# Performance work log

Hardware: AMD Instinct MI355X
Metric: run time of the kernel (lower is better)

The kernel has to match this reference:

```python
import jax, jax.numpy as jnp
import numpy as np

SR = 4  # search_range
D = 2 * SR + 1  # 9
NC = D * D      # 81 output channels


def setup_inputs() -> dict:
    key = jax.random.key(0)
    k1, k2 = jax.random.split(key)
    B, C, H, W = 8, 64, 192, 256
    x1 = jax.random.normal(k1, (B, C, H, W), dtype=jnp.float32)
    x2 = jax.random.normal(k2, (B, C, H, W), dtype=jnp.float32)
    return {"x1": x1, "x2": x2}


def reference(x1, x2):
    B, C, H, W = x1.shape
    # Zero-pad x2 so out-of-overlap products are zero, matching the
    # zero-initialized cv in the original module.
    x2p = jnp.pad(x2, ((0, 0), (0, 0), (SR, SR), (SR, SR)))
    outs = [None] * NC
    for i in range(-SR, SR + 1):
        for j in range(-SR, SR + 1):
            # Original torch code uses cv[:, 9*i + j] with negative wraparound.
            k = (D * i + j) % NC
            # x2 sample position is (h - i, w - j); in padded coords start = SR - i.
            shifted = jax.lax.dynamic_slice(
                x2p, (0, 0, SR - i, SR - j), (B, C, H, W))
            outs[k] = jnp.sum(x1 * shifted, axis=1)  # [B, H, W]
    cv = jnp.stack(outs, axis=1)  # [B, 81, H, W]
    return cv / NC
```

## Files before the change

kernel.cpp:

```cpp
#include <hip/hip_runtime.h>

#define HH 192
#define WW 256
#define TH 8
#define TW 32
#define CCH 4
#define NCHUNK 16
#define THREADS 576
#define CHSTEP (CCH * HH * WW)

typedef float f4 __attribute__((ext_vector_type(4)));

#define GLL(gp, lp) __builtin_amdgcn_global_load_lds(                        \
    (const __attribute__((address_space(1))) unsigned int*)(gp),            \
    (__attribute__((address_space(3))) unsigned int*)(lp), 16, 0, 0)

__global__ __launch_bounds__(THREADS) void cost_volume_kernel(
    const float* __restrict__ x1, const float* __restrict__ x2,
    float* __restrict__ out)
{
    __shared__ __align__(16) float smem[7168];

    const int tid  = threadIdx.x;
    const int wave = tid >> 6;
    const int lane = tid & 63;
    const int r    = lane >> 3;
    const int wcg  = lane & 7;

    const int bid = blockIdx.x;
    const int b   = bid / 192;
    const int rem = bid % 192;
    const int h0  = (rem >> 3) * TH;
    const int w0  = (rem & 7) * TW;

    const int u2a = tid;
    const int ch2a = u2a / 160, r2a = (u2a % 160) / 10, c2a = (u2a % 10) * 4;
    const int hg2a = h0 - 4 + r2a, wg2a = w0 - 4 + c2a;
    const bool v2a = (hg2a >= 0) & (hg2a < HH) & (wg2a >= 0) & (wg2a <= WW - 4);
    const long off2a = ((long)(b * 64 + ch2a) * HH + hg2a) * WW + wg2a;

    const int u2b = 576 + lane;
    const int ch2b = u2b / 160, r2b = (u2b % 160) / 10, c2b = (u2b % 10) * 4;
    const int hg2b = h0 - 4 + r2b, wg2b = w0 - 4 + c2b;
    const bool v2b = (wave == 0) & (hg2b >= 0) & (hg2b < HH) &
                     (wg2b >= 0) & (wg2b <= WW - 4);
    const long off2b = ((long)(b * 64 + ch2b) * HH + hg2b) * WW + wg2b;

    const bool hx1 = (wave >= 1) & (wave <= 4);
    const int u1 = (64 * (wave - 1) + lane) & 255;
    const int ch1 = u1 >> 6, r1 = (u1 & 63) >> 3, c1 = (u1 & 7) * 4;
    const long off1 = ((long)(b * 64 + ch1) * HH + (h0 + r1)) * WW + (w0 + c1);

    auto issue = [&](int nb, int n) {
        const long cofs = (long)n * CHSTEP;
        float* const l2a = smem + 2048 + nb * 2560 + 256 * wave;
        float* const l2b = smem + 2048 + nb * 2560 + 2304;
        float* const l1  = smem + nb * 1024 + 256 * (wave - 1);
        if (v2a) GLL(x2 + off2a + cofs, l2a);
        if (v2b) GLL(x2 + off2b + cofs, l2b);
        if (hx1) GLL(x1 + off1 + cofs, l1);
    };

    const f4 z4 = {0.f, 0.f, 0.f, 0.f};
    for (int z = tid; z < 7168 / 4; z += THREADS) ((f4*)smem)[z] = z4;
    __syncthreads();

    issue(0, 0);
    __syncthreads();

    f4 acc0 = z4, acc1 = z4, acc2 = z4, acc3 = z4, acc4 = z4,
       acc5 = z4, acc6 = z4, acc7 = z4, acc8 = z4;

    const int row2 = r + 8 - wave;

    for (int n = 0; n < NCHUNK; ++n) {
        if (n + 1 < NCHUNK) issue((n + 1) & 1, n + 1);
        const float* sb1 = smem + (n & 1) * 1024 + r * 32 + wcg * 4;
        const float* sb2 = smem + 2048 + (n & 1) * 2560 + row2 * 40 + wcg * 4;
#pragma unroll
        for (int cc = 0; cc < CCH; ++cc) {
            const f4 av  = *(const f4*)(sb1 + cc * 256);
            const f4 xv0 = *(const f4*)(sb2 + cc * 640);
            const f4 xv1 = *(const f4*)(sb2 + cc * 640 + 4);
            const f4 xv2 = *(const f4*)(sb2 + cc * 640 + 8);
            const f4 w8 = xv0;
            const f4 w7 = __builtin_shufflevector(xv0, xv1, 1, 2, 3, 4);
            const f4 w6 = __builtin_shufflevector(xv0, xv1, 2, 3, 4, 5);
            const f4 w5 = __builtin_shufflevector(xv0, xv1, 3, 4, 5, 6);
            const f4 w4 = xv1;
            const f4 w3 = __builtin_shufflevector(xv1, xv2, 1, 2, 3, 4);
            const f4 w2 = __builtin_shufflevector(xv1, xv2, 2, 3, 4, 5);
            const f4 w1 = __builtin_shufflevector(xv1, xv2, 3, 4, 5, 6);
            const f4 w0 = xv2;
            acc0 = __builtin_elementwise_fma(av, w0, acc0);
            acc1 = __builtin_elementwise_fma(av, w1, acc1);
            acc2 = __builtin_elementwise_fma(av, w2, acc2);
            acc3 = __builtin_elementwise_fma(av, w3, acc3);
            acc4 = __builtin_elementwise_fma(av, w4, acc4);
            acc5 = __builtin_elementwise_fma(av, w5, acc5);
            acc6 = __builtin_elementwise_fma(av, w6, acc6);
            acc7 = __builtin_elementwise_fma(av, w7, acc7);
            acc8 = __builtin_elementwise_fma(av, w8, acc8);
        }
        __syncthreads();
    }

    const float scale = 1.0f / 81.0f;
    const int hout = h0 + r;
    const int wout = w0 + wcg * 4;
#define CV_OUT(JJ)                                                           \
    {                                                                        \
        const int k = (9 * wave + (JJ) + 41) % 81;                           \
        float* po = out + (((long)b * 81 + k) * HH + hout) * WW + wout;      \
        *(f4*)po = acc##JJ * scale;                                          \
    }
    CV_OUT(0) CV_OUT(1) CV_OUT(2) CV_OUT(3) CV_OUT(4)
    CV_OUT(5) CV_OUT(6) CV_OUT(7) CV_OUT(8)
#undef CV_OUT
}

extern "C" void kernel_launch(void* const* d_in, const int* in_sizes, int n_in,
                              void* d_out, int out_size, void* d_ws, size_t ws_size,
                              hipStream_t stream) {
    const float* x1 = (const float*)d_in[0];
    const float* x2 = (const float*)d_in[1];
    float* out = (float*)d_out;
    dim3 grid(8 * 24 * 8);
    dim3 block(THREADS);
    hipLaunchKernelGGL(cost_volume_kernel, grid, block, 0, stream, x1, x2, out);
}
```

Baseline: 120.7 us.

## Load x1 directly into registers and double channel chunk size

Stops staging x1 through LDS; each thread now reads its own x1 float4 straight from global memory into registers, and LDS holds only x2 halos. The channel chunk per pipeline stage doubles from 4 to 8, which halves the number of barriers and enlarges the x2 LDS buffers. This aims to cut LDS traffic and synchronisation overhead. The cost is direct global loads that sit on the compute critical path, plus more LDS per block, which may lower occupancy.

```diff
diff --git a/kernel.cpp b/kernel.cpp
--- a/kernel.cpp
+++ b/kernel.cpp
@@ -4,8 +4,8 @@
 #define WW 256
 #define TH 8
 #define TW 32
-#define CCH 4
-#define NCHUNK 16
+#define CCH 8
+#define NCHUNK 8
 #define THREADS 576
 #define CHSTEP (CCH * HH * WW)
 
@@ -19,7 +19,7 @@
     const float* __restrict__ x1, const float* __restrict__ x2,
     float* __restrict__ out)
 {
-    __shared__ __align__(16) float smem[7168];
+    __shared__ __align__(16) float smem[10240];
 
     const int tid  = threadIdx.x;
     const int wave = tid >> 6;
@@ -33,36 +33,33 @@
     const int h0  = (rem >> 3) * TH;
     const int w0  = (rem & 7) * TW;
 
-    const int u2a = tid;
-    const int ch2a = u2a / 160, r2a = (u2a % 160) / 10, c2a = (u2a % 10) * 4;
-    const int hg2a = h0 - 4 + r2a, wg2a = w0 - 4 + c2a;
-    const bool v2a = (hg2a >= 0) & (hg2a < HH) & (wg2a >= 0) & (wg2a <= WW - 4);
-    const long off2a = ((long)(b * 64 + ch2a) * HH + hg2a) * WW + wg2a;
+    const int uA = tid;
+    const int uB = 576 + tid;
+    const int uC = 1152 + tid;
+    const bool hC = (tid < 128);
 
-    const int u2b = 576 + lane;
-    const int ch2b = u2b / 160, r2b = (u2b % 160) / 10, c2b = (u2b % 10) * 4;
-    const int hg2b = h0 - 4 + r2b, wg2b = w0 - 4 + c2b;
-    const bool v2b = (wave == 0) & (hg2b >= 0) & (hg2b < HH) &
-                     (wg2b >= 0) & (wg2b <= WW - 4);
-    const long off2b = ((long)(b * 64 + ch2b) * HH + hg2b) * WW + wg2b;
-
-    const bool hx1 = (wave >= 1) & (wave <= 4);
-    const int u1 = (64 * (wave - 1) + lane) & 255;
-    const int ch1 = u1 >> 6, r1 = (u1 & 63) >> 3, c1 = (u1 & 7) * 4;
-    const long off1 = ((long)(b * 64 + ch1) * HH + (h0 + r1)) * WW + (w0 + c1);
+    auto desc = [&](int u, bool& v, long& goff) {
+        const int ch = u / 160, row = (u % 160) / 10, c4 = (u % 10) * 4;
+        const int hg = h0 - 4 + row, wg = w0 - 4 + c4;
+        v = (hg >= 0) & (hg < HH) & (wg >= 0) & (wg <= WW - 4);
+        goff = ((long)(b * 64 + ch) * HH + hg) * WW + wg;
+    };
+    bool vA, vB, vC0; long gA, gB, gC;
+    desc(uA, vA, gA);
+    desc(uB, vB, gB);
+    desc(uC, vC0, gC);
+    const bool vC = vC0 & hC;
 
     auto issue = [&](int nb, int n) {
         const long cofs = (long)n * CHSTEP;
-        float* const l2a = smem + 2048 + nb * 2560 + 256 * wave;
-        float* const l2b = smem + 2048 + nb * 2560 + 2304;
-        float* const l1  = smem + nb * 1024 + 256 * (wave - 1);
-        if (v2a) GLL(x2 + off2a + cofs, l2a);
-        if (v2b) GLL(x2 + off2b + cofs, l2b);
-        if (hx1) GLL(x1 + off1 + cofs, l1);
+        float* const base = smem + nb * 5120;
+        if (vA) GLL(x2 + gA + cofs, base + 256 * wave);
+        if (vB) GLL(x2 + gB + cofs, base + 2304 + 256 * wave);
+        if (vC) GLL(x2 + gC + cofs, base + 4608 + 256 * wave);
     };
 
     const f4 z4 = {0.f, 0.f, 0.f, 0.f};
-    for (int z = tid; z < 7168 / 4; z += THREADS) ((f4*)smem)[z] = z4;
+    for (int z = tid; z < 10240 / 4; z += THREADS) ((f4*)smem)[z] = z4;
     __syncthreads();
 
     issue(0, 0);
@@ -72,36 +69,55 @@
        acc5 = z4, acc6 = z4, acc7 = z4, acc8 = z4;
 
     const int row2 = r + 8 - wave;
+    const float* x1p = x1 + ((long)(b * 64) * HH + (h0 + r)) * WW + w0 + wcg * 4;
 
     for (int n = 0; n < NCHUNK; ++n) {
         if (n + 1 < NCHUNK) issue((n + 1) & 1, n + 1);
-        const float* sb1 = smem + (n & 1) * 1024 + r * 32 + wcg * 4;
-        const float* sb2 = smem + 2048 + (n & 1) * 2560 + row2 * 40 + wcg * 4;
-#pragma unroll
-        for (int cc = 0; cc < CCH; ++cc) {
-            const f4 av  = *(const f4*)(sb1 + cc * 256);
-            const f4 xv0 = *(const f4*)(sb2 + cc * 640);
-            const f4 xv1 = *(const f4*)(sb2 + cc * 640 + 4);
-            const f4 xv2 = *(const f4*)(sb2 + cc * 640 + 8);
-            const f4 w8 = xv0;
-            const f4 w7 = __builtin_shufflevector(xv0, xv1, 1, 2, 3, 4);
-            const f4 w6 = __builtin_shufflevector(xv0, xv1, 2, 3, 4, 5);
-            const f4 w5 = __builtin_shufflevector(xv0, xv1, 3, 4, 5, 6);
-            const f4 w4 = xv1;
-            const f4 w3 = __builtin_shufflevector(xv1, xv2, 1, 2, 3, 4);
-            const f4 w2 = __builtin_shufflevector(xv1, xv2, 2, 3, 4, 5);
-            const f4 w1 = __builtin_shufflevector(xv1, xv2, 3, 4, 5, 6);
-            const f4 w0 = xv2;
-            acc0 = __builtin_elementwise_fma(av, w0, acc0);
-            acc1 = __builtin_elementwise_fma(av, w1, acc1);
-            acc2 = __builtin_elementwise_fma(av, w2, acc2);
-            acc3 = __builtin_elementwise_fma(av, w3, acc3);
-            acc4 = __builtin_elementwise_fma(av, w4, acc4);
-            acc5 = __builtin_elementwise_fma(av, w5, acc5);
-            acc6 = __builtin_elementwise_fma(av, w6, acc6);
-            acc7 = __builtin_elementwise_fma(av, w7, acc7);
-            acc8 = __builtin_elementwise_fma(av, w8, acc8);
+        const float* sb2 = smem + (n & 1) * 5120 + row2 * 40 + wcg * 4;
+        const float* x1c = x1p + (long)n * CHSTEP;
+
+#define CV_CC(CC, AV)                                                        \
+        {                                                                    \
+            const f4 xv0 = *(const f4*)(sb2 + (CC) * 640);                   \
+            const f4 xv1 = *(const f4*)(sb2 + (CC) * 640 + 4);               \
+            const f4 xv2 = *(const f4*)(sb2 + (CC) * 640 + 8);               \
+            const f4 w8 = xv0;                                               \
+            const f4 w7 = __builtin_shufflevector(xv0, xv1, 1, 2, 3, 4);     \
+            const f4 w6 = __builtin_shufflevector(xv0, xv1, 2, 3, 4, 5);     \
+            const f4 w5 = __builtin_shufflevector(xv0, xv1, 3, 4, 5, 6);     \
+            const f4 w4 = xv1;                                               \
+            const f4 w3 = __builtin_shufflevector(xv1, xv2, 1, 2, 3, 4);     \
+            const f4 w2 = __builtin_shufflevector(xv1, xv2, 2, 3, 4, 5);     \
+            const f4 w1 = __builtin_shufflevector(xv1, xv2, 3, 4, 5, 6);     \
+            const f4 w0 = xv2;                                               \
+            acc0 = __builtin_elementwise_fma(AV, w0, acc0);                  \
+            acc1 = __builtin_elementwise_fma(AV, w1, acc1);                  \
+            acc2 = __builtin_elementwise_fma(AV, w2, acc2);                  \
+            acc3 = __builtin_elementwise_fma(AV, w3, acc3);                  \
+            acc4 = __builtin_elementwise_fma(AV, w4, acc4);                  \
+            acc5 = __builtin_elementwise_fma(AV, w5, acc5);                  \
+            acc6 = __builtin_elementwise_fma(AV, w6, acc6);                  \
+            acc7 = __builtin_elementwise_fma(AV, w7, acc7);                  \
+            acc8 = __builtin_elementwise_fma(AV, w8, acc8);                  \
         }
+
+        const f4 a0 = *(const f4*)(x1c);
+        const f4 a1 = *(const f4*)(x1c + 1 * (HH * WW));
+        const f4 a2 = *(const f4*)(x1c + 2 * (HH * WW));
+        const f4 a3 = *(const f4*)(x1c + 3 * (HH * WW));
+        CV_CC(0, a0)
+        CV_CC(1, a1)
+        const f4 a4 = *(const f4*)(x1c + 4 * (HH * WW));
+        const f4 a5 = *(const f4*)(x1c + 5 * (HH * WW));
+        const f4 a6 = *(const f4*)(x1c + 6 * (HH * WW));
+        const f4 a7 = *(const f4*)(x1c + 7 * (HH * WW));
+        CV_CC(2, a2)
+        CV_CC(3, a3)
+        CV_CC(4, a4)
+        CV_CC(5, a5)
+        CV_CC(6, a6)
+        CV_CC(7, a7)
+#undef CV_CC
         __syncthreads();
     }
 
```

Measured after the change: 145.8 us. +20.9%, slower.
